# Kernel optimization log

Hardware: AMD Instinct MI355X
Metric: run time of the kernel (lower is better)

The kernel has to match this reference:

```python
import jax, jax.numpy as jnp
import numpy as np

RADII = (0.4, 0.8, 1.2)
SIGMA2 = 2.0 * 0.2 ** 2   # Gaussian shell-density bandwidth
ALPHA = 0.3               # keras LeakyReLU default
EPS = 1e-3                # keras BatchNormalization default epsilon


def _n_coeffs(L):
    return sum((2 * l + 1) ** 2 for l in range(L + 1))


def _pullback_idx(L):
    # flat index of Wigner block entry (m, n=0) for each SH coeff (l, m)
    idx, off = [], 0
    for l in range(L + 1):
        d = 2 * l + 1
        idx += [off + m * d + l for m in range(d)]
        off += d * d
    return np.asarray(idx, dtype=np.int32)


def setup_inputs() -> dict:
    key = jax.random.key(0)
    ks = jax.random.split(key, 20)
    B, N, Q, S = 64, 2048, 1024, 512
    T = [_n_coeffs(l) for l in (5, 4, 3)]  # 286, 165, 84
    f32 = jnp.float32

    def nrm(k, shape, scale=1.0):
        return jax.random.normal(ks[k], shape, dtype=f32) * scale

    dirs = nrm(1, (3, S, 3))
    dirs = dirs / jnp.linalg.norm(dirs, axis=-1, keepdims=True)
    z = lambda n: jnp.zeros((n,), f32)
    o = lambda n: jnp.ones((n,), f32)
    return {
        "x": nrm(0, (B, N, 3)),
        "shell_dirs": dirs,                                   # [3, 512, 3]
        "A_sh": nrm(2, (36, S), 1.0 / np.sqrt(S)),            # SH projection (l_max=5)
        "D_eval0": nrm(3, (Q, T[0]), 1.0 / np.sqrt(T[0])),    # Wigner eval bases
        "D_eval1": nrm(4, (Q, T[1]), 1.0 / np.sqrt(T[1])),
        "D_eval2": nrm(5, (Q, T[2]), 1.0 / np.sqrt(T[2])),
        "D_coef1": nrm(6, (T[1], Q), 1.0 / np.sqrt(Q)),       # Wigner coeff (projection) bases
        "D_coef2": nrm(7, (T[2], Q), 1.0 / np.sqrt(Q)),
        "D_coef_last": nrm(8, (T[2], Q), 1.0 / np.sqrt(Q)),
        "W0": nrm(9, (3, 16), 1.0 / np.sqrt(3)), "b0": z(16),
        "W1": nrm(10, (16, 32), 0.25), "b1": z(32),
        "W2": nrm(11, (32, 64), 1.0 / np.sqrt(32)), "b2": z(64),
        "g0": o(16), "be0": z(16),
        "g1": o(32), "be1": z(32),
        "g2": o(64), "be2": z(64),
        "Wfc1": nrm(12, (256, 512), 1.0 / 16.0), "bfc1": z(512),
        "gfc1": o(512), "befc1": z(512),
        "Wfc2": nrm(13, (512, 256), 1.0 / np.sqrt(512)), "bfc2": z(256),
        "gfc2": o(256), "befc2": z(256),
        "Wout": nrm(14, (256, 40), 1.0 / 16.0), "bout": z(40),
    }


def _bn(y, g, b, axes):
    m = jnp.mean(y, axis=axes, keepdims=True)
    v = jnp.var(y, axis=axes, keepdims=True)
    return (y - m) * jax.lax.rsqrt(v + EPS) * g + b


def reference(x, shell_dirs, A_sh, D_eval0, D_eval1, D_eval2,
              D_coef1, D_coef2, D_coef_last,
              W0, b0, W1, b1, W2, b2,
              g0, be0, g1, be1, g2, be2,
              Wfc1, bfc1, gfc1, befc1, Wfc2, bfc2, gfc2, befc2,
              Wout, bout):
    B = x.shape[0]
    # --- sphere_shell_embedding: Gaussian shell density -> SH coeffs per shell ---
    xn2 = jnp.sum(x * x, -1)[..., None]                 # [B,N,1]
    sh = []
    for i, r in enumerate(RADII):
        c = r * shell_dirs[i]                           # [S,3]
        d2 = xn2 + jnp.sum(c * c, -1) - 2.0 * (x @ c.T)  # [B,N,S]
        f = jnp.mean(jnp.exp(-d2 / SIGMA2), axis=1)      # [B,S]
        sh.append(f @ A_sh.T)                            # [B,36]
    sh = jnp.stack(sh, axis=-1)                          # [B,36,3] shells as channels
    # --- S2_to_SO3_pullback: Y_lm -> D^l_{m,0} column of Wigner blocks ---
    idx = jnp.asarray(_pullback_idx(5))
    y = jnp.zeros((B, 286, 3), sh.dtype).at[:, idx, :].set(sh)
    # --- layer 0: SO3Conv (per-coeff channel mix) + WignerEval + BN + LReLU + WignerCoeffs ---
    y = jnp.einsum('btc,cu->btu', y, W0) + b0
    y = jnp.einsum('qt,btu->bqu', D_eval0, y)            # [B,1024,16]
    y = jax.nn.leaky_relu(_bn(y, g0, be0, (0, 1)), ALPHA)
    y = jnp.einsum('tq,bqu->btu', D_coef1, y)            # [B,165,16]
    # --- layer 1 ---
    y = jnp.einsum('btc,cu->btu', y, W1) + b1
    y = jnp.einsum('qt,btu->bqu', D_eval1, y)            # [B,1024,32]
    y = jax.nn.leaky_relu(_bn(y, g1, be1, (0, 1)), ALPHA)
    y = jnp.einsum('tq,bqu->btu', D_coef2, y)            # [B,84,32]
    # --- layer 2 ---
    y = jnp.einsum('btc,cu->btu', y, W2) + b2
    y = jnp.einsum('qt,btu->bqu', D_eval2, y)            # [B,1024,64]
    y = jax.nn.leaky_relu(_bn(y, g2, be2, (0, 1)), ALPHA)
    y = jnp.einsum('tq,bqu->btu', D_coef_last, y)        # [B,84,64]
    # --- degree-wise norms (rotation-invariant pooling), l_max=3 blocks ---
    offs, sizes = (0, 1, 10, 35), (1, 9, 25, 49)
    feats = jnp.concatenate(
        [jnp.linalg.norm(y[:, o:o + s, :], axis=1, keepdims=True)
         for o, s in zip(offs, sizes)], axis=1)          # [B,4,64]
    h = feats.reshape(B, -1)                             # [B,256]
    # --- MLP head (dropout = identity at inference) ---
    h = jax.nn.relu(_bn(h @ Wfc1 + bfc1, gfc1, befc1, (0,)))
    h = jax.nn.relu(_bn(h @ Wfc2 + bfc2, gfc2, befc2, (0,)))
    return jax.nn.softmax(h @ Wout + bout, axis=-1)
```

## Files before the change

### kernel.cpp

```cpp
#include <hip/hip_runtime.h>
#include <hip/hip_bf16.h>

#define BB 64
#define NN 2048
#define QQ 1024
#define SS 512
#define NCH 16
#define PREPB 609
#define QKN3 4

__device__ const int PIDX[36] = {
    0, 2, 5, 8, 12, 17, 22, 27, 32, 38, 45, 52, 59, 66, 73, 80,
    88, 97, 106, 115, 124, 133, 142, 151, 160,
    170, 181, 192, 203, 214, 225, 236, 247, 258, 269, 280};

__global__ __launch_bounds__(256) void k_preshell(
    const float* __restrict__ De0, const float* __restrict__ De1, const float* __restrict__ De2,
    float* __restrict__ Dg0t, float* __restrict__ rs0,
    float* __restrict__ Det1, float* __restrict__ Det2,
    float* __restrict__ stats,
    const float* __restrict__ x, const float* __restrict__ dirs, float* __restrict__ pbuf) {
    __shared__ float tile[32][33];
    __shared__ float4 lx[NN / NCH];
    int blk = blockIdx.x, tid = threadIdx.x;
    if (blk < PREPB) {
        int r = tid >> 5, c = tid & 31;
        if (blk < 192) {
            int tq = blk & 31, tt = blk >> 5;
            int q0 = tq * 32, t0 = tt * 32;
            for (int rr = r; rr < 32; rr += 8) {
                int t = t0 + c;
                tile[rr][c] = (t < 165) ? De1[(q0 + rr) * 165 + t] : 0.f;
            }
            __syncthreads();
            for (int rr = r; rr < 32; rr += 8) {
                int t = t0 + rr;
                if (t < 165) Det1[t * QQ + q0 + c] = tile[c][rr];
            }
        } else if (blk < 288) {
            int i = blk - 192;
            int tq = i & 31, tt = i >> 5;
            int q0 = tq * 32, t0 = tt * 32;
            for (int rr = r; rr < 32; rr += 8) {
                int t = t0 + c;
                tile[rr][c] = (t < 84) ? De2[(q0 + rr) * 84 + t] : 0.f;
            }
            __syncthreads();
            for (int rr = r; rr < 32; rr += 8) {
                int t = t0 + rr;
                if (t < 84) Det2[t * QQ + q0 + c] = tile[c][rr];
            }
        } else if (blk < 352) {
            int i = blk - 288;
            int tq = i & 31, tj = i >> 5;
            int q0 = tq * 32, j0 = tj * 32;
            for (int rr = r; rr < 32; rr += 8) {
                int j = j0 + c;
                tile[rr][c] = (j < 36) ? De0[(q0 + rr) * 286 + PIDX[j]] : 0.f;
            }
            __syncthreads();
            for (int rr = r; rr < 32; rr += 8) {
                int j = j0 + rr;
                if (j < 36) Dg0t[j * QQ + q0 + c] = tile[c][rr];
            }
        } else if (blk < 608) {
            int w = tid >> 6, lane = tid & 63;
            int q = (blk - 352) * 4 + w;
            float s = 0.f;
#pragma unroll
            for (int p = 0; p < 5; p++) {
                int idx = lane + p * 64;
                if (idx < 286) s += De0[q * 286 + idx];
            }
#pragma unroll
            for (int o = 32; o > 0; o >>= 1) s += __shfl_xor(s, o, 64);
            if (lane == 0) rs0[q] = s;
        } else {
            if (tid < 224) stats[tid] = 0.f;
        }
        return;
    }
    int idx = blk - PREPB;
    int b = idx & 63, zc = idx >> 6;
    const float KL = 18.033688011112042f;
    const float* xb = x + ((size_t)b * NN + zc * (NN / NCH)) * 3;
    for (int n = tid; n < NN / NCH; n += 256) {
        float X = xb[n * 3 + 0];
        float Y = xb[n * 3 + 1];
        float Z = xb[n * 3 + 2];
        lx[n] = make_float4(X, Y, Z, -KL * (X * X + Y * Y + Z * Z));
    }
    __syncthreads();
    float cxs[3][2], cys[3][2], czs[3][2], bas[3][2];
#pragma unroll
    for (int i = 0; i < 3; i++) {
        float r = (i == 0) ? 0.4f : ((i == 1) ? 0.8f : 1.2f);
#pragma unroll
        for (int h = 0; h < 2; h++) {
            int s = tid + h * 256;
            float cx = r * dirs[(i * SS + s) * 3 + 0];
            float cy = r * dirs[(i * SS + s) * 3 + 1];
            float cz = r * dirs[(i * SS + s) * 3 + 2];
            bas[i][h] = -KL * (cx * cx + cy * cy + cz * cz);
            cxs[i][h] = 2.f * KL * cx;
            cys[i][h] = 2.f * KL * cy;
            czs[i][h] = 2.f * KL * cz;
        }
    }
    float acc[3][2][2];
#pragma unroll
    for (int i = 0; i < 3; i++)
#pragma unroll
        for (int h = 0; h < 2; h++) { acc[i][h][0] = 0.f; acc[i][h][1] = 0.f; }
#pragma unroll 2
    for (int n = 0; n < NN / NCH; n += 2) {
        float4 p0 = lx[n];
        float4 p1 = lx[n + 1];
#pragma unroll
        for (int i = 0; i < 3; i++)
#pragma unroll
            for (int h = 0; h < 2; h++) {
                acc[i][h][0] += __builtin_amdgcn_exp2f(
                    fmaf(cxs[i][h], p0.x, fmaf(cys[i][h], p0.y, fmaf(czs[i][h], p0.z, p0.w + bas[i][h]))));
                acc[i][h][1] += __builtin_amdgcn_exp2f(
                    fmaf(cxs[i][h], p1.x, fmaf(cys[i][h], p1.y, fmaf(czs[i][h], p1.z, p1.w + bas[i][h]))));
            }
    }
#pragma unroll
    for (int i = 0; i < 3; i++) {
        float* o = pbuf + ((size_t)(zc * 3 + i) * BB + b) * SS;
        o[tid] = acc[i][0][0] + acc[i][0][1];
        o[tid + 256] = acc[i][1][0] + acc[i][1][1];
    }
}

__global__ __launch_bounds__(256) void k_eval0(const float* __restrict__ pbuf,
                                               const float* __restrict__ A_sh,
                                               const float* __restrict__ W0,
                                               const float* __restrict__ b0,
                                               const float* __restrict__ Dg0t,
                                               const float* __restrict__ rs0,
                                               float* __restrict__ yq, float* __restrict__ stats) {
    __shared__ float lf[3][SS];
    __shared__ float lsh[36][3];
    __shared__ float llm[576];
    __shared__ float lred[4][32];
    int qc = blockIdx.x, b = blockIdx.y, tid = threadIdx.x;
    for (int i = tid; i < 3 * SS; i += 256) {
        int c = i / SS, s = i % SS;
        float v = 0.f;
#pragma unroll
        for (int zc = 0; zc < NCH; zc++) v += pbuf[((size_t)(zc * 3 + c) * BB + b) * SS + s];
        lf[c][s] = v * (1.0f / NN);
    }
    __syncthreads();
    int w = tid >> 6, lane = tid & 63;
    for (int p = w; p < 108; p += 4) {
        int j = p / 3, c = p % 3;
        const float* As = A_sh + j * SS;
        float a = 0.f;
#pragma unroll
        for (int k = 0; k < 8; k++) a = fmaf(lf[c][lane + 64 * k], As[lane + 64 * k], a);
#pragma unroll
        for (int o = 32; o > 0; o >>= 1) a += __shfl_xor(a, o, 64);
        if (lane == 0) lsh[j][c] = a;
    }
    __syncthreads();
    for (int i = tid; i < 576; i += 256) {
        int j = i >> 4, u = i & 15;
        float m = 0.f;
#pragma unroll
        for (int c = 0; c < 3; c++) m = fmaf(lsh[j][c], W0[c * 16 + u], m);
        llm[i] = m;
    }
    __syncthreads();
    int q = qc * 256 + tid;
    float acc[16];
#pragma unroll
    for (int u = 0; u < 16; u++) acc[u] = 0.f;
#pragma unroll 4
    for (int j = 0; j < 36; j++) {
        float d = Dg0t[j * QQ + q];
#pragma unroll
        for (int u = 0; u < 16; u++) acc[u] = fmaf(d, llm[j * 16 + u], acc[u]);
    }
    float rb = rs0[q];
#pragma unroll
    for (int u = 0; u < 16; u++) acc[u] = fmaf(b0[u], rb, acc[u]);
#pragma unroll
    for (int u = 0; u < 16; u++) yq[((size_t)b * 16 + u) * QQ + q] = acc[u];
#pragma unroll
    for (int u = 0; u < 16; u++) {
        float v = acc[u], v2 = acc[u] * acc[u];
#pragma unroll
        for (int o = 32; o > 0; o >>= 1) {
            v += __shfl_xor(v, o, 64);
            v2 += __shfl_xor(v2, o, 64);
        }
        if (lane == 0) { lred[w][u] = v; lred[w][16 + u] = v2; }
    }
    __syncthreads();
    if (tid < 32) atomicAdd(&stats[tid], lred[0][tid] + lred[1][tid] + lred[2][tid] + lred[3][tid]);
}

template <int TT, int UU, int QKN>
__global__ __launch_bounds__(256) void k_coefG(const float* __restrict__ yq,
                                               const float* __restrict__ Dc,
                                               const float* __restrict__ stats,
                                               const float* __restrict__ g,
                                               const float* __restrict__ be,
                                               float* __restrict__ part) {
    constexpr int KC = QQ / QKN;
    __shared__ float lA[32][68];
    __shared__ float lB[32][68];
    __shared__ float lsu[UU], ltu[UU];
    int mt = blockIdx.x, nt = blockIdx.y, qk = blockIdx.z, tid = threadIdx.x;
    int m0 = mt * 64, n0 = nt * 64, k0 = qk * KC;
    if (tid < UU) {
        const float inv = 1.0f / (BB * QQ);
        float mm = stats[tid] * inv;
        float var = stats[UU + tid] * inv - mm * mm;
        float s = g[tid] * rsqrtf(fmaxf(var, 0.f) + 1e-3f);
        lsu[tid] = s;
        ltu[tid] = be[tid] - mm * s;
    }
    __syncthreads();
    int r = tid >> 2, f = (tid & 3) * 4;
    bool mok = (m0 + r) < TT;
    const float* arow = Dc + (size_t)(mok ? (m0 + r) : 0) * QQ;
    const float* brow = yq + (size_t)(n0 + r) * QQ;
    float su = lsu[(n0 + r) % UU], tu = ltu[(n0 + r) % UU];
    int tg = tid >> 4, ug = tid & 15;
    float acc[4][4];
#pragma unroll
    for (int i = 0; i < 4; i++)
#pragma unroll
        for (int j = 0; j < 4; j++) acc[i][j] = 0.f;
    for (int kb = 0; kb < KC; kb += 32) {
        int kg = k0 + kb;
#pragma unroll
        for (int p = 0; p < 2; p++) {
            int ko = f + p * 16;
            float4 a4 = make_float4(0.f, 0.f, 0.f, 0.f);
            if (mok) a4 = *(const float4*)(arow + kg + ko);
            float4 b4 = *(const float4*)(brow + kg + ko);
#pragma unroll
            for (int i = 0; i < 4; i++) {
                float v = fmaf((&b4.x)[i], su, tu);
                lA[ko + i][r] = (&a4.x)[i];
                lB[ko + i][r] = (v > 0.f) ? v : 0.3f * v;
            }
        }
        __syncthreads();
#pragma unroll 2
        for (int kk = 0; kk < 32; kk++) {
            float4 a4 = *(const float4*)&lA[kk][tg * 4];
            float4 b4 = *(const float4*)&lB[kk][ug * 4];
#pragma unroll
            for (int i = 0; i < 4; i++) {
                float av = (&a4.x)[i];
                acc[i][0] = fmaf(av, b4.x, acc[i][0]);
                acc[i][1] = fmaf(av, b4.y, acc[i][1]);
                acc[i][2] = fmaf(av, b4.z, acc[i][2]);
                acc[i][3] = fmaf(av, b4.w, acc[i][3]);
            }
        }
        __syncthreads();
    }
    int n = n0 + ug * 4;
    int b = n / UU, u0 = n % UU;
#pragma unroll
    for (int i = 0; i < 4; i++) {
        int t = m0 + tg * 4 + i;
        if (t < TT)
            *(float4*)&part[(((size_t)qk * BB + b) * TT + t) * UU + u0] =
                make_float4(acc[i][0], acc[i][1], acc[i][2], acc[i][3]);
    }
}

template <int TT, int CC, int UU, int QKN, int TTp, int TS>
__global__ __launch_bounds__(256) void k_redmix(const float* __restrict__ part,
                                                const float* __restrict__ W,
                                                const float* __restrict__ bias,
                                                float* __restrict__ ym) {
    constexpr int TSL = TTp / TS;
    __shared__ float lyt[TSL][CC + 1];
    int b = blockIdx.x, ts = blockIdx.y, tid = threadIdx.x;
    int t0 = ts * TSL;
    for (int i = tid; i < TSL * CC; i += 256) {
        int tl = i / CC, c = i % CC;
        int t = t0 + tl;
        float v = 0.f;
        if (t < TT) {
#pragma unroll
            for (int k = 0; k < QKN; k++)
                v += part[(size_t)k * (BB * TT * CC) + ((size_t)b * TT + t) * CC + c];
        }
        lyt[tl][c] = v;
    }
    __syncthreads();
    for (int i = tid; i < UU * TSL; i += 256) {
        int u = i / TSL, tl = i % TSL;
        int t = t0 + tl;
        float m = 0.f;
        if (t < TT) {
            m = bias[u];
#pragma unroll
            for (int c = 0; c < CC; c++) m = fmaf(lyt[tl][c], W[c * UU + u], m);
        }
        ym[((size_t)b * UU + u) * TTp + t] = m;
    }
}

template <int TT, int TTp, int UU>
__global__ __launch_bounds__(256) void k_evalG(const float* __restrict__ ym,
                                               const float* __restrict__ Det,
                                               float* __restrict__ yq,
                                               float* __restrict__ stats) {
    __shared__ float lA[32][68];
    __shared__ float lB[32][68];
    __shared__ float sred[2][64];
    int mt = blockIdx.x, qt = blockIdx.y, tid = threadIdx.x;
    int m0 = mt * 64, q0 = qt * 64;
    int r = tid >> 2, f = (tid & 3) * 4;
    const float* arow = ym + (size_t)(m0 + r) * TTp;
    int br = tid >> 4, bq = (tid & 15) * 4;
    int tg = tid >> 4, ug = tid & 15;
    float acc[4][4];
#pragma unroll
    for (int i = 0; i < 4; i++)
#pragma unroll
        for (int j = 0; j < 4; j++) acc[i][j] = 0.f;
    for (int kb = 0; kb < TT; kb += 32) {
#pragma unroll
        for (int p = 0; p < 2; p++) {
            int ko = f + p * 16;
            float4 a4 = *(const float4*)(arow + kb + ko);
#pragma unroll
            for (int i = 0; i < 4; i++) lA[ko + i][r] = (&a4.x)[i];
            int kk = br + p * 16;
            int t = kb + kk;
            float4 b4 = make_float4(0.f, 0.f, 0.f, 0.f);
            if (t < TT) b4 = *(const float4*)(Det + (size_t)t * QQ + q0 + bq);
            *(float4*)&lB[kk][bq] = b4;
        }
        __syncthreads();
#pragma unroll 2
        for (int kk = 0; kk < 32; kk++) {
            float4 a4 = *(const float4*)&lA[kk][tg * 4];
            float4 b4 = *(const float4*)&lB[kk][ug * 4];
#pragma unroll
            for (int i = 0; i < 4; i++) {
                float av = (&a4.x)[i];
                acc[i][0] = fmaf(av, b4.x, acc[i][0]);
                acc[i][1] = fmaf(av, b4.y, acc[i][1]);
                acc[i][2] = fmaf(av, b4.z, acc[i][2]);
                acc[i][3] = fmaf(av, b4.w, acc[i][3]);
            }
        }
        __syncthreads();
    }
    float s1[4], s2[4];
#pragma unroll
    for (int i = 0; i < 4; i++) {
        int m = m0 + tg * 4 + i;
        *(float4*)&yq[(size_t)m * QQ + q0 + ug * 4] =
            make_float4(acc[i][0], acc[i][1], acc[i][2], acc[i][3]);
        s1[i] = (acc[i][0] + acc[i][1]) + (acc[i][2] + acc[i][3]);
        s2[i] = fmaf(acc[i][0], acc[i][0], fmaf(acc[i][1], acc[i][1],
                 fmaf(acc[i][2], acc[i][2], acc[i][3] * acc[i][3])));
    }
#pragma unroll
    for (int o = 1; o < 16; o <<= 1) {
#pragma unroll
        for (int i = 0; i < 4; i++) {
            s1[i] += __shfl_xor(s1[i], o, 64);
            s2[i] += __shfl_xor(s2[i], o, 64);
        }
    }
    if (ug == 0) {
#pragma unroll
        for (int i = 0; i < 4; i++) {
            sred[0][tg * 4 + i] = s1[i];
            sred[1][tg * 4 + i] = s2[i];
        }
    }
    __syncthreads();
    if (tid < 2 * UU) {
        int which = tid / UU, u = tid % UU;
        float s = 0.f;
        for (int rr = u; rr < 64; rr += UU) s += sred[which][rr];
        atomicAdd(&stats[which * UU + u], s);
    }
}

__global__ __launch_bounds__(256) void k_norms(const float* __restrict__ part, float* __restrict__ ht0) {
    __shared__ float red[4][64];
    int b = blockIdx.x, blk = blockIdx.y;
    int tq = threadIdx.x >> 6, u = threadIdx.x & 63;
    const int offs[4] = {0, 1, 10, 35};
    const int ends[4] = {1, 10, 35, 84};
    float a = 0.f;
    for (int t = offs[blk] + tq; t < ends[blk]; t += 4) {
        float v = 0.f;
#pragma unroll
        for (int k = 0; k < QKN3; k++)
            v += part[(size_t)k * (BB * 84 * 64) + (b * 84 + t) * 64 + u];
        a = fmaf(v, v, a);
    }
    red[tq][u] = a;
    __syncthreads();
    if (tq == 0) {
        float s = red[0][u] + red[1][u] + red[2][u] + red[3][u];
        ht0[(blk * 64 + u) * BB + b] = sqrtf(fmaxf(s, 0.f));
    }
}

template <int K, int J>
__global__ __launch_bounds__(512) void k_fc(const float* __restrict__ in, const float* __restrict__ W,
                                            const float* __restrict__ bias, const float* __restrict__ g,
                                            const float* __restrict__ be, float* __restrict__ out) {
    __shared__ float red[8][64];
    int j = blockIdx.x;
    int b = threadIdx.x & 63, kq = threadIdx.x >> 6;
    constexpr int KS = K / 8;
    int kbeg = kq * KS;
    float a0 = 0.f, a1 = 0.f, a2 = 0.f, a3 = 0.f;
#pragma unroll 4
    for (int k = kbeg; k < kbeg + KS; k += 4) {
        a0 = fmaf(in[k * BB + b], W[(size_t)k * J + j], a0);
        a1 = fmaf(in[(k + 1) * BB + b], W[(size_t)(k + 1) * J + j], a1);
        a2 = fmaf(in[(k + 2) * BB + b], W[(size_t)(k + 2) * J + j], a2);
        a3 = fmaf(in[(k + 3) * BB + b], W[(size_t)(k + 3) * J + j], a3);
    }
    red[kq][b] = (a0 + a1) + (a2 + a3);
    __syncthreads();
    if (kq == 0) {
        float acc = bias[j];
#pragma unroll
        for (int i = 0; i < 8; i++) acc += red[i][b];
        float s1 = acc, s2 = acc * acc;
#pragma unroll
        for (int o = 32; o > 0; o >>= 1) {
            s1 += __shfl_xor(s1, o, 64);
            s2 += __shfl_xor(s2, o, 64);
        }
        float m = s1 * (1.0f / 64.f);
        float var = s2 * (1.0f / 64.f) - m * m;
        float sc = g[j] * rsqrtf(fmaxf(var, 0.f) + 1e-3f);
        float v = (acc - m) * sc + be[j];
        out[j * BB + b] = fmaxf(v, 0.f);
    }
}

__global__ __launch_bounds__(256) void k_out(const float* __restrict__ ht2, const float* __restrict__ Wout,
                                             const float* __restrict__ bout, float* __restrict__ outp) {
    __shared__ float red[4][64];
    __shared__ float sm[64];
    int b = blockIdx.x;
    int o = threadIdx.x & 63, kq = threadIdx.x >> 6;
    float a0 = 0.f, a1 = 0.f, a2 = 0.f, a3 = 0.f;
    int kbeg = kq * 64;
    if (o < 40) {
#pragma unroll 4
        for (int k = kbeg; k < kbeg + 64; k += 4) {
            a0 = fmaf(ht2[k * BB + b], Wout[k * 40 + o], a0);
            a1 = fmaf(ht2[(k + 1) * BB + b], Wout[(k + 1) * 40 + o], a1);
            a2 = fmaf(ht2[(k + 2) * BB + b], Wout[(k + 2) * 40 + o], a2);
            a3 = fmaf(ht2[(k + 3) * BB + b], Wout[(k + 3) * 40 + o], a3);
        }
    }
    red[kq][o] = (a0 + a1) + (a2 + a3);
    __syncthreads();
    if (kq == 0) {
        float acc = red[0][o] + red[1][o] + red[2][o] + red[3][o] + ((o < 40) ? bout[o] : 0.f);
        sm[o] = (o < 40) ? acc : -3.0e38f;
        __syncthreads();
        for (int s = 32; s > 0; s >>= 1) {
            if (o < s) sm[o] = fmaxf(sm[o], sm[o + s]);
            __syncthreads();
        }
        float m = sm[0];
        __syncthreads();
        const float L2E = 1.4426950408889634f;
        float e = (o < 40) ? exp2f((acc - m) * L2E) : 0.f;
        sm[o] = e;
        __syncthreads();
        for (int s = 32; s > 0; s >>= 1) {
            if (o < s) sm[o] += sm[o + s];
            __syncthreads();
        }
        if (o < 40) outp[b * 40 + o] = e / sm[0];
    }
}

#define OFF_PBUF 0
#define OFF_DG0T 1572864
#define OFF_RS0 1609728
#define OFF_DET1 1610752
#define OFF_DET2 1779712
#define OFF_YQ 1865728
#define OFF_YM 6060032
#define OFF_HT0 6453248
#define OFF_HT1 6469632
#define OFF_HT2 6502400
#define OFF_STATS 6518784

extern "C" void kernel_launch(void* const* d_in, const int* in_sizes, int n_in,
                              void* d_out, int out_size, void* d_ws, size_t ws_size,
                              hipStream_t stream) {
    const float* x = (const float*)d_in[0];
    const float* shell_dirs = (const float*)d_in[1];
    const float* A_sh = (const float*)d_in[2];
    const float* D_eval0 = (const float*)d_in[3];
    const float* D_eval1 = (const float*)d_in[4];
    const float* D_eval2 = (const float*)d_in[5];
    const float* D_coef1 = (const float*)d_in[6];
    const float* D_coef2 = (const float*)d_in[7];
    const float* D_coef_last = (const float*)d_in[8];
    const float* W0 = (const float*)d_in[9];
    const float* b0 = (const float*)d_in[10];
    const float* W1 = (const float*)d_in[11];
    const float* b1 = (const float*)d_in[12];
    const float* W2 = (const float*)d_in[13];
    const float* b2 = (const float*)d_in[14];
    const float* g0 = (const float*)d_in[15];
    const float* be0 = (const float*)d_in[16];
    const float* g1 = (const float*)d_in[17];
    const float* be1 = (const float*)d_in[18];
    const float* g2 = (const float*)d_in[19];
    const float* be2 = (const float*)d_in[20];
    const float* Wfc1 = (const float*)d_in[21];
    const float* bfc1 = (const float*)d_in[22];
    const float* gfc1 = (const float*)d_in[23];
    const float* befc1 = (const float*)d_in[24];
    const float* Wfc2 = (const float*)d_in[25];
    const float* bfc2 = (const float*)d_in[26];
    const float* gfc2 = (const float*)d_in[27];
    const float* befc2 = (const float*)d_in[28];
    const float* Wout = (const float*)d_in[29];
    const float* bout = (const float*)d_in[30];
    float* out = (float*)d_out;

    float* ws = (float*)d_ws;
    float* pbuf = ws + OFF_PBUF;
    float* part = ws + OFF_PBUF;
    float* Dg0t = ws + OFF_DG0T;
    float* rs0 = ws + OFF_RS0;
    float* Det1 = ws + OFF_DET1;
    float* Det2 = ws + OFF_DET2;
    float* yq = ws + OFF_YQ;
    float* ym = ws + OFF_YM;
    float* ht0 = ws + OFF_HT0;
    float* ht1 = ws + OFF_HT1;
    float* ht2 = ws + OFF_HT2;
    float* stats = ws + OFF_STATS;
    float* stats0 = stats;
    float* stats1 = stats + 32;
    float* stats2 = stats + 96;

    k_preshell<<<PREPB + BB * NCH, 256, 0, stream>>>(
        D_eval0, D_eval1, D_eval2, Dg0t, rs0, Det1, Det2, stats, x, shell_dirs, pbuf);
    k_eval0<<<dim3(4, BB), 256, 0, stream>>>(pbuf, A_sh, W0, b0, Dg0t, rs0, yq, stats0);
    k_coefG<165, 16, 8><<<dim3(3, 16, 8), 256, 0, stream>>>(yq, D_coef1, stats0, g0, be0, part);
    k_redmix<165, 16, 32, 8, 192, 8><<<dim3(BB, 8), 256, 0, stream>>>(part, W1, b1, ym);
    k_evalG<165, 192, 32><<<dim3(32, 16), 256, 0, stream>>>(ym, Det1, yq, stats1);
    k_coefG<84, 32, 8><<<dim3(2, 32, 8), 256, 0, stream>>>(yq, D_coef2, stats1, g1, be1, part);
    k_redmix<84, 32, 64, 8, 96, 8><<<dim3(BB, 8), 256, 0, stream>>>(part, W2, b2, ym);
    k_evalG<84, 96, 64><<<dim3(64, 16), 256, 0, stream>>>(ym, Det2, yq, stats2);
    k_coefG<84, 64, QKN3><<<dim3(2, 64, QKN3), 256, 0, stream>>>(yq, D_coef_last, stats2, g2, be2, part);
    k_norms<<<dim3(BB, 4), 256, 0, stream>>>(part, ht0);
    k_fc<256, 512><<<512, 512, 0, stream>>>(ht0, Wfc1, bfc1, gfc1, befc1, ht1);
    k_fc<512, 256><<<256, 512, 0, stream>>>(ht1, Wfc2, bfc2, gfc2, befc2, ht2);
    k_out<<<BB, 256, 0, stream>>>(ht2, Wout, bout, out);
}
```

Baseline: 331.2 us.

## Split SH projection into its own kernel and raise last coefficient split

The per-batch spherical-harmonic projection (summing shell partials and dotting with A_sh) is moved out of k_eval0 into a new k_sh kernel over (batch, channel, half), so the four q-chunk blocks of k_eval0 no longer each redo the reduction. The shell-density inner loop is simplified to a single accumulator per shell with unroll 4. The final coefficient kernel's q-split goes from 4 to 8, and partial buffers get dedicated workspace regions instead of aliasing pbuf. This adds one kernel launch and a small intermediate buffer.

After: 312.5 us. 5.6% less time.

```diff
diff --git a/kernel.cpp b/kernel.cpp
--- a/kernel.cpp
+++ b/kernel.cpp
@@ -7,7 +7,7 @@
 #define SS 512
 #define NCH 16
 #define PREPB 609
-#define QKN3 4
+#define QKN3 8
 
 __device__ const int PIDX[36] = {
     0, 2, 5, 8, 12, 17, 22, 27, 32, 38, 45, 52, 59, 66, 73, 80,
@@ -107,63 +107,63 @@
             czs[i][h] = 2.f * KL * cz;
         }
     }
-    float acc[3][2][2];
-#pragma unroll
-    for (int i = 0; i < 3; i++)
-#pragma unroll
-        for (int h = 0; h < 2; h++) { acc[i][h][0] = 0.f; acc[i][h][1] = 0.f; }
-#pragma unroll 2
-    for (int n = 0; n < NN / NCH; n += 2) {
-        float4 p0 = lx[n];
-        float4 p1 = lx[n + 1];
+    float acc[3][2];
+#pragma unroll
+    for (int i = 0; i < 3; i++) { acc[i][0] = 0.f; acc[i][1] = 0.f; }
+#pragma unroll 4
+    for (int n = 0; n < NN / NCH; n++) {
+        float4 p = lx[n];
 #pragma unroll
         for (int i = 0; i < 3; i++)
 #pragma unroll
-            for (int h = 0; h < 2; h++) {
-                acc[i][h][0] += __builtin_amdgcn_exp2f(
-                    fmaf(cxs[i][h], p0.x, fmaf(cys[i][h], p0.y, fmaf(czs[i][h], p0.z, p0.w + bas[i][h]))));
-                acc[i][h][1] += __builtin_amdgcn_exp2f(
-                    fmaf(cxs[i][h], p1.x, fmaf(cys[i][h], p1.y, fmaf(czs[i][h], p1.z, p1.w + bas[i][h]))));
-            }
+            for (int h = 0; h < 2; h++)
+                acc[i][h] += __builtin_amdgcn_exp2f(
+                    fmaf(cxs[i][h], p.x, fmaf(cys[i][h], p.y, fmaf(czs[i][h], p.z, p.w + bas[i][h]))));
     }
 #pragma unroll
     for (int i = 0; i < 3; i++) {
         float* o = pbuf + ((size_t)(zc * 3 + i) * BB + b) * SS;
-        o[tid] = acc[i][0][0] + acc[i][0][1];
-        o[tid + 256] = acc[i][1][0] + acc[i][1][1];
-    }
-}
-
-__global__ __launch_bounds__(256) void k_eval0(const float* __restrict__ pbuf,
-                                               const float* __restrict__ A_sh,
+        o[tid] = acc[i][0];
+        o[tid + 256] = acc[i][1];
+    }
+}
+
+__global__ __launch_bounds__(256) void k_sh(const float* __restrict__ pbuf,
+                                            const float* __restrict__ A_sh,
+                                            float* __restrict__ lshp) {
+    __shared__ float lf[256];
+    int b = blockIdx.x, c = blockIdx.y, h = blockIdx.z, tid = threadIdx.x;
+    float v = 0.f;
+#pragma unroll
+    for (int zc = 0; zc < NCH; zc++)
+        v += pbuf[((size_t)(zc * 3 + c) * BB + b) * SS + h * 256 + tid];
+    lf[tid] = v * (1.0f / NN);
+    __syncthreads();
+    int w = tid >> 6, lane = tid & 63;
+    for (int j = w; j < 36; j += 4) {
+        const float* As = A_sh + j * SS + h * 256;
+        float a = 0.f;
+#pragma unroll
+        for (int k = 0; k < 4; k++) a = fmaf(lf[lane + 64 * k], As[lane + 64 * k], a);
+#pragma unroll
+        for (int o = 32; o > 0; o >>= 1) a += __shfl_xor(a, o, 64);
+        if (lane == 0) lshp[((b * 36 + j) * 3 + c) * 2 + h] = a;
+    }
+}
+
+__global__ __launch_bounds__(256) void k_eval0(const float* __restrict__ lshp,
                                                const float* __restrict__ W0,
                                                const float* __restrict__ b0,
                                                const float* __restrict__ Dg0t,
                                                const float* __restrict__ rs0,
                                                float* __restrict__ yq, float* __restrict__ stats) {
-    __shared__ float lf[3][SS];
     __shared__ float lsh[36][3];
     __shared__ float llm[576];
     __shared__ float lred[4][32];
     int qc = blockIdx.x, b = blockIdx.y, tid = threadIdx.x;
-    for (int i = tid; i < 3 * SS; i += 256) {
-        int c = i / SS, s = i % SS;
-        float v = 0.f;
-#pragma unroll
-        for (int zc = 0; zc < NCH; zc++) v += pbuf[((size_t)(zc * 3 + c) * BB + b) * SS + s];
-        lf[c][s] = v * (1.0f / NN);
-    }
-    __syncthreads();
-    int w = tid >> 6, lane = tid & 63;
-    for (int p = w; p < 108; p += 4) {
-        int j = p / 3, c = p % 3;
-        const float* As = A_sh + j * SS;
-        float a = 0.f;
-#pragma unroll
-        for (int k = 0; k < 8; k++) a = fmaf(lf[c][lane + 64 * k], As[lane + 64 * k], a);
-#pragma unroll
-        for (int o = 32; o > 0; o >>= 1) a += __shfl_xor(a, o, 64);
-        if (lane == 0) lsh[j][c] = a;
+    if (tid < 108) {
+        int j = tid / 3, c = tid % 3;
+        lsh[j][c] = lshp[((b * 36 + j) * 3 + c) * 2 + 0] + lshp[((b * 36 + j) * 3 + c) * 2 + 1];
     }
     __syncthreads();
     for (int i = tid; i < 576; i += 256) {
@@ -189,6 +189,7 @@
     for (int u = 0; u < 16; u++) acc[u] = fmaf(b0[u], rb, acc[u]);
 #pragma unroll
     for (int u = 0; u < 16; u++) yq[((size_t)b * 16 + u) * QQ + q] = acc[u];
+    int lane = tid & 63, w = tid >> 6;
 #pragma unroll
     for (int u = 0; u < 16; u++) {
         float v = acc[u], v2 = acc[u] * acc[u];
@@ -501,10 +502,13 @@
 #define OFF_DET2 1779712
 #define OFF_YQ 1865728
 #define OFF_YM 6060032
-#define OFF_HT0 6453248
-#define OFF_HT1 6469632
-#define OFF_HT2 6502400
-#define OFF_STATS 6518784
+#define OFF_LSH 6453248
+#define OFF_HT0 6467072
+#define OFF_HT1 6483456
+#define OFF_HT2 6516224
+#define OFF_STATS 6532608
+#define OFF_PART 6532864
+#define OFF_PART3 7909120
 
 extern "C" void kernel_launch(void* const* d_in, const int* in_sizes, int n_in,
                               void* d_out, int out_size, void* d_ws, size_t ws_size,
@@ -544,32 +548,35 @@
 
     float* ws = (float*)d_ws;
     float* pbuf = ws + OFF_PBUF;
-    float* part = ws + OFF_PBUF;
     float* Dg0t = ws + OFF_DG0T;
     float* rs0 = ws + OFF_RS0;
     float* Det1 = ws + OFF_DET1;
     float* Det2 = ws + OFF_DET2;
     float* yq = ws + OFF_YQ;
     float* ym = ws + OFF_YM;
+    float* lshp = ws + OFF_LSH;
     float* ht0 = ws + OFF_HT0;
     float* ht1 = ws + OFF_HT1;
     float* ht2 = ws + OFF_HT2;
     float* stats = ws + OFF_STATS;
+    float* part = ws + OFF_PART;
+    float* part3 = ws + OFF_PART3;
     float* stats0 = stats;
     float* stats1 = stats + 32;
     float* stats2 = stats + 96;
 
     k_preshell<<<PREPB + BB * NCH, 256, 0, stream>>>(
         D_eval0, D_eval1, D_eval2, Dg0t, rs0, Det1, Det2, stats, x, shell_dirs, pbuf);
-    k_eval0<<<dim3(4, BB), 256, 0, stream>>>(pbuf, A_sh, W0, b0, Dg0t, rs0, yq, stats0);
+    k_sh<<<dim3(BB, 3, 2), 256, 0, stream>>>(pbuf, A_sh, lshp);
+    k_eval0<<<dim3(4, BB), 256, 0, stream>>>(lshp, W0, b0, Dg0t, rs0, yq, stats0);
     k_coefG<165, 16, 8><<<dim3(3, 16, 8), 256, 0, stream>>>(yq, D_coef1, stats0, g0, be0, part);
     k_redmix<165, 16, 32, 8, 192, 8><<<dim3(BB, 8), 256, 0, stream>>>(part, W1, b1, ym);
     k_evalG<165, 192, 32><<<dim3(32, 16), 256, 0, stream>>>(ym, Det1, yq, stats1);
     k_coefG<84, 32, 8><<<dim3(2, 32, 8), 256, 0, stream>>>(yq, D_coef2, stats1, g1, be1, part);
     k_redmix<84, 32, 64, 8, 96, 8><<<dim3(BB, 8), 256, 0, stream>>>(part, W2, b2, ym);
     k_evalG<84, 96, 64><<<dim3(64, 16), 256, 0, stream>>>(ym, Det2, yq, stats2);
-    k_coefG<84, 64, QKN3><<<dim3(2, 64, QKN3), 256, 0, stream>>>(yq, D_coef_last, stats2, g2, be2, part);
-    k_norms<<<dim3(BB, 4), 256, 0, stream>>>(part, ht0);
+    k_coefG<84, 64, QKN3><<<dim3(2, 64, QKN3), 256, 0, stream>>>(yq, D_coef_last, stats2, g2, be2, part3);
+    k_norms<<<dim3(BB, 4), 256, 0, stream>>>(part3, ht0);
     k_fc<256, 512><<<512, 512, 0, stream>>>(ht0, Wfc1, bfc1, gfc1, befc1, ht1);
     k_fc<512, 256><<<256, 512, 0, stream>>>(ht1, Wfc2, bfc2, gfc2, befc2, ht2);
     k_out<<<BB, 256, 0, stream>>>(ht2, Wout, bout, out);
```
